# Performance work log

Hardware: AMD Instinct MI355X
Metric: run time of the kernel (lower is better)

## Reference

```python
import math
import jax, jax.numpy as jnp
import numpy as np

B, H, V, DEPTH = 8, 1024, 32000, 14
LN_EPS = 1e-5


def _structure(depth):
    """Replicates recurse()/expand() index bookkeeping. Pure python, static.
    Returns per-level boolean masks (len 2K, interleaved left/right per parent),
    B_l/B_r of the root, and sibling pair list S, in the exact original order."""
    def rec(idx_start, n, lengths):
        K = len(lengths)
        idxs = list(range(idx_start, idx_start + K))
        B_l = [[i] for i in idxs]
        B_r = [[i] for i in idxs]
        if n > 1:
            pmask = [(L - 1) > 0 for L in lengths]
            mask, child_lengths = [], []
            for L, m in zip(lengths, pmask):
                mask += [m, m]
                if m:
                    child_lengths += [math.ceil((L - 1) ** 0.75), L - 1]
            masks_below, lB_l, lB_r, S = rec(idxs[-1] + 1, n - 1, child_lengths)
            masks = [np.array(mask, dtype=bool)] + masks_below
            j = 0
            for i in range(K):
                if pmask[i]:
                    B_l[i].extend(lB_l[j])
                    B_r[i].extend(lB_r[j + 1])
                    for v_i in lB_r[j]:
                        for v_j in lB_l[j + 1]:
                            S.append((v_i, v_j))
                    j += 2
        else:
            masks, S = [], []
        return masks, B_l, B_r, S

    masks, B_l, B_r, S = rec(0, depth, [depth])
    return masks, B_l[0], B_r[0], S


def setup_inputs() -> dict:
    key = jax.random.key(0)
    ks = jax.random.split(key, 8)
    s = 0.02  # weight scale for numerical sanity
    return {
        'x': jax.random.normal(ks[0], (B, H), jnp.float32),
        'W_in': jax.random.normal(ks[1], (H, H), jnp.float32) * s,
        'b_in': jnp.zeros((H,), jnp.float32),
        'W_g': jax.random.normal(ks[2], (H, H), jnp.float32) * s,
        'b_g': jnp.zeros((H,), jnp.float32),
        'W_cell': jax.random.normal(ks[3], (2 * H, 2 * H), jnp.float32) * s,
        'b_cell': jnp.zeros((2 * H,), jnp.float32),
        'ln_g': jnp.ones((H,), jnp.float32),
        'ln_b': jnp.zeros((H,), jnp.float32),
        'W_leaf': jax.random.normal(ks[4], (H, 2), jnp.float32) * s,
        'b_leaf': jnp.zeros((2,), jnp.float32),
        'W_out': jax.random.normal(ks[5], (H, V), jnp.float32) * s,
        'b_out': jnp.zeros((V,), jnp.float32),
        'depth': DEPTH,
    }


def _layernorm(z, g, b):
    mu = z.mean(-1, keepdims=True)
    var = ((z - mu) ** 2).mean(-1, keepdims=True)
    return (z - mu) * jax.lax.rsqrt(var + LN_EPS) * g + b


def reference(x, W_in, b_in, W_g, b_g, W_cell, b_cell, ln_g, ln_b,
              W_leaf, b_leaf, W_out, b_out, depth):
    masks, Bl0, Br0, S = _structure(int(depth))
    h_dim = x.shape[-1]

    g = x @ W_g + b_g                                     # global_transform, [B,H]
    prev_h = (x @ W_in + b_in)[None]                      # init_parent, [1,B,H]
    prev_ll = jax.nn.log_softmax(prev_h @ W_leaf + b_leaf, axis=-1)  # [1,B,2]

    hs, ls = [prev_h], [prev_ll]
    for mask in masks:                                    # depth-1 static levels
        K, Bb = prev_h.shape[0], prev_h.shape[1]
        inp = jnp.concatenate([prev_h, jnp.broadcast_to(g, prev_h.shape)], axis=-1)
        z = (inp @ W_cell + b_cell).reshape(K, Bb, 2, h_dim)
        branches = jnp.tanh(_layernorm(z, ln_g, ln_b))    # cell: two child states
        log_leaf = jax.nn.log_softmax(branches @ W_leaf + b_leaf, axis=-1)
        ltl = 0.5 * prev_ll[:, :, None, 1:] + log_leaf    # update_logbreak
        fb = branches.transpose(0, 2, 1, 3).reshape(2 * K, Bb, h_dim)  # flatten_struct
        fl = ltl.transpose(0, 2, 1, 3).reshape(2 * K, Bb, 2)
        sel = np.nonzero(mask)[0]                         # static gather indices
        prev_h, prev_ll = fb[sel], fl[sel]
        hs.append(prev_h)
        ls.append(prev_ll)

    hiddens = jnp.concatenate(hs, axis=0)                 # [T,B,H]
    leaves = jnp.concatenate(ls, axis=0)                  # [T,B,2]
    log_words = jax.nn.log_softmax(hiddens @ W_out + b_out, axis=-1)  # [T,B,V]

    start_idxs = jnp.asarray(np.array(Bl0, dtype=np.int32))
    end_idxs = jnp.asarray(np.array(Br0, dtype=np.int32))
    Sarr = np.array(S, dtype=np.int32).reshape(-1, 2)
    out_idxs = jnp.asarray(Sarr[:, 0])
    in_idxs = jnp.asarray(Sarr[:, 1])
    return log_words, leaves, start_idxs, end_idxs, out_idxs, in_idxs
```

## Files before the change

### kernel.cpp

```cpp
#include <hip/hip_runtime.h>
#include <cstdint>
#include <cstddef>


typedef __attribute__((ext_vector_type(4))) float   f4;
typedef __attribute__((ext_vector_type(4))) float   f32x4;
typedef __attribute__((ext_vector_type(8))) __bf16  bf16x8;
typedef __attribute__((ext_vector_type(4))) unsigned short us4;
typedef __attribute__((ext_vector_type(8))) unsigned short us8;

constexpr int DEPTH = 14;
constexpr int Bb = 8;
constexpr int Hd = 1024;
constexpr int Vv = 32000;
constexpr int NT = Vv / 128;
constexpr int MAXT = 512;
constexpr int MAXS = 4096;
constexpr int MAXP = 32;
constexpr float L2E = 1.44269504088896340736f;

struct SB {
  int lvlOff[DEPTH + 1];
  int lvlK[DEPTH];
  int len[MAXT];
  int lch[MAXT], rch[MAXT];
  int parCnt[DEPTH];
  int parRows[DEPTH][MAXP];
  int T;
  int nS;
  int sOut[MAXS], sIn[MAXS];
  int nStart, nEnd;
  int startIdx[16], endIdx[16];
};

constexpr int ceil75(int L) {
  constexpr int t[14] = {0, 1, 2, 3, 3, 4, 4, 5, 5, 6, 6, 7, 7, 7};
  return t[L];
}

constexpr SB build() {
  SB s{};
  for (int i = 0; i < MAXT; i++) { s.lch[i] = -1; s.rch[i] = -1; }
  s.lvlOff[0] = 0; s.lvlK[0] = 1; s.len[0] = DEPTH;
  for (int l = 0; l < DEPTH - 1; l++) {
    int off = s.lvlOff[l], K = s.lvlK[l];
    int nxt = off + K, cnt = 0;
    for (int i = 0; i < K; i++) {
      int g = off + i;
      if (s.len[g] > 1) {
        int gl = nxt + 2 * cnt, gr = gl + 1;
        s.lch[g] = gl; s.rch[g] = gr;
        s.len[gl] = ceil75(s.len[g] - 1);
        s.len[gr] = s.len[g] - 1;
        s.parRows[l][cnt] = g;
        cnt++;
      }
    }
    s.parCnt[l] = cnt;
    s.lvlOff[l + 1] = nxt;
    s.lvlK[l + 1] = 2 * cnt;
  }
  s.T = s.lvlOff[DEPTH - 1] + s.lvlK[DEPTH - 1];
  s.nS = 0;
  for (int l = DEPTH - 2; l >= 0; l--) {
    for (int pi = 0; pi < s.parCnt[l]; pi++) {
      int g = s.parRows[l][pi];
      for (int u = s.lch[g]; u != -1; u = s.rch[u])
        for (int v = s.rch[g]; v != -1; v = s.lch[v]) {
          s.sOut[s.nS] = u; s.sIn[s.nS] = v; s.nS++;
        }
    }
  }
  s.nStart = 0;
  for (int u = 0; u != -1; u = s.lch[u]) s.startIdx[s.nStart++] = u;
  s.nEnd = 0;
  for (int u = 0; u != -1; u = s.rch[u]) s.endIdx[s.nEnd++] = u;
  return s;
}

constexpr SB HS = build();
__device__ const SB DS = build();

struct PR { int v[MAXP]; };

__device__ __forceinline__ unsigned short f2bf(float f) {
  union { float f; unsigned u; } v; v.f = f;
  unsigned r = v.u + 0x7fffu + ((v.u >> 16) & 1u);
  return (unsigned short)(r >> 16);
}

__global__ void k_wout_t(const float* __restrict__ Wout,
                         unsigned short* __restrict__ Wt) {
  __shared__ float t[64][129];
  int tid = threadIdx.x;
  int n0 = blockIdx.x * 128, k0 = blockIdx.y * 64;
#pragma unroll
  for (int i = 0; i < 8; i++) {
    int k = (tid >> 5) + 8 * i;
    int c = (tid & 31) * 4;
    f4 v = *(const f4*)&Wout[(size_t)(k0 + k) * Vv + n0 + c];
    t[k][c] = v.x; t[k][c + 1] = v.y; t[k][c + 2] = v.z; t[k][c + 3] = v.w;
  }
  __syncthreads();
#pragma unroll
  for (int pass = 0; pass < 4; pass++) {
    int n = (tid >> 3) + 32 * pass;
    int ks = (tid & 7) * 8;
    us8 o;
#pragma unroll
    for (int q = 0; q < 8; q++) o[q] = f2bf(t[ks + q][n]);
    *(us8*)&Wt[(size_t)(n0 + n) * Hd + k0 + ks] = o;
  }
}

__global__ void k_wct(const float* __restrict__ Wc,
                      unsigned short* __restrict__ Wct) {
  __shared__ float t[32][33];
  int tx = threadIdx.x, ty = threadIdx.y;
  int n0 = blockIdx.x * 32, k0 = blockIdx.y * 32;
  for (int i = 0; i < 4; i++)
    t[ty + 8 * i][tx] = Wc[(size_t)(k0 + ty + 8 * i) * 2048 + n0 + tx];
  __syncthreads();
  for (int i = 0; i < 4; i++)
    Wct[(size_t)(n0 + ty + 8 * i) * Hd + k0 + tx] = f2bf(t[tx][ty + 8 * i]);
}

__global__ void k_init(const float* __restrict__ x, const float* __restrict__ Wg,
                       const float* __restrict__ bg, const float* __restrict__ Win,
                       const float* __restrict__ bin, float* __restrict__ gbuf,
                       float* __restrict__ hidd, unsigned short* __restrict__ hiddb) {
  __shared__ float xs[Bb * Hd];
  __shared__ float part[Bb][128];
  int tid = threadIdx.x;
  int mat = blockIdx.y;
  const float* W = mat ? Win : Wg;
  const float* bias = mat ? bin : bg;
  for (int i = tid; i < Bb * Hd; i += 256) xs[i] = x[i];
  __syncthreads();
  int c = tid & 127, kh = tid >> 7;
  int col = blockIdx.x * 128 + c;
  float acc[Bb];
#pragma unroll
  for (int b = 0; b < Bb; b++) acc[b] = 0.f;
  for (int k = kh * 512; k < kh * 512 + 512; k++) {
    float w = W[(size_t)k * Hd + col];
#pragma unroll
    for (int b = 0; b < Bb; b++) acc[b] += xs[b * Hd + k] * w;
  }
  if (kh == 1)
    for (int b = 0; b < Bb; b++) part[b][c] = acc[b];
  __syncthreads();
  if (kh == 0) {
    for (int b = 0; b < Bb; b++) {
      float v = acc[b] + part[b][c] + bias[col];
      if (mat == 0) gbuf[b * Hd + col] = v;
      else { hidd[(size_t)b * Hd + col] = v; hiddb[(size_t)b * Hd + col] = f2bf(v); }
    }
  }
}

__global__ void k_gw(const float* __restrict__ gbuf, const float* __restrict__ Wc,
                     const float* __restrict__ bc, float* __restrict__ gW) {
  __shared__ float xs[Bb * Hd];
  __shared__ float part[Bb][128];
  int tid = threadIdx.x;
  for (int i = tid; i < Bb * Hd; i += 256) xs[i] = gbuf[i];
  __syncthreads();
  int c = tid & 127, kh = tid >> 7;
  int col = blockIdx.x * 128 + c;
  float acc[Bb];
#pragma unroll
  for (int b = 0; b < Bb; b++) acc[b] = 0.f;
  for (int k = kh * 512; k < kh * 512 + 512; k++) {
    float w = Wc[(size_t)(Hd + k) * 2048 + col];
#pragma unroll
    for (int b = 0; b < Bb; b++) acc[b] += xs[b * Hd + k] * w;
  }
  if (kh == 1)
    for (int b = 0; b < Bb; b++) part[b][c] = acc[b];
  __syncthreads();
  if (kh == 0)
    for (int b = 0; b < Bb; b++)
      gW[(size_t)b * 2048 + col] = acc[b] + part[b][c] + bc[col];
}

__global__ void k_leaf0(const float* __restrict__ hidd, const float* __restrict__ Wl,
                        const float* __restrict__ bl, float* __restrict__ leaves) {
  int b = threadIdx.x >> 6, lane = threadIdx.x & 63;
  float d0 = 0.f, d1 = 0.f;
  for (int k = lane; k < Hd; k += 64) {
    float h = hidd[(size_t)b * Hd + k];
    d0 += h * Wl[2 * k];
    d1 += h * Wl[2 * k + 1];
  }
  for (int off = 32; off; off >>= 1) {
    d0 += __shfl_down(d0, off);
    d1 += __shfl_down(d1, off);
  }
  if (lane == 0) {
    float l0 = d0 + bl[0], l1 = d1 + bl[1];
    float m = fmaxf(l0, l1);
    float L = logf(expf(l0 - m) + expf(l1 - m));
    leaves[b * 2 + 0] = l0 - m - L;
    leaves[b * 2 + 1] = l1 - m - L;
  }
}

__global__ __launch_bounds__(256) void k_cellg(
    const unsigned short* __restrict__ A, const unsigned short* __restrict__ Bt,
    float* __restrict__ zbuf, PR pr, int Mtot) {
  __shared__ short As[128 * 64];
  __shared__ short Bs[128 * 64];
  int tid = threadIdx.x;
  int lane = tid & 63, w = tid >> 6;
  int wm = w & 1, wn = w >> 1;
  int R0 = blockIdx.x * 128, C0 = blockIdx.y * 128;
  int ks = blockIdx.z;
  f32x4 acc[4][4];
#pragma unroll
  for (int i = 0; i < 4; i++)
#pragma unroll
    for (int j = 0; j < 4; j++) acc[i][j] = 0.f;
  int quad = lane >> 4, l15 = lane & 15;
  int srow = lane >> 3;
  int kc = lane & 7;
  for (int kb = ks * 4; kb < ks * 4 + 4; kb++) {
    int k0 = kb * 64;
#pragma unroll
    for (int i = 0; i < 4; i++) {
      int rowb = w * 32 + i * 8;
      int m = rowb + srow;
      int kcx = kc ^ (m & 7);
      int gr = R0 + m;
      int grc = gr < Mtot ? gr : 0;
      int arow = pr.v[grc >> 3] * Bb + (grc & 7);
      const unsigned short* ga = A + (size_t)arow * Hd + k0 + kcx * 8;
      const unsigned short* gb = Bt + (size_t)(C0 + m) * Hd + k0 + kcx * 8;
      __builtin_amdgcn_global_load_lds(
          (__attribute__((address_space(1))) void*)ga,
          (__attribute__((address_space(3))) void*)&As[rowb * 64], 16, 0, 0);
      __builtin_amdgcn_global_load_lds(
          (__attribute__((address_space(1))) void*)gb,
          (__attribute__((address_space(3))) void*)&Bs[rowb * 64], 16, 0, 0);
    }
    __syncthreads();
#pragma unroll
    for (int ksi = 0; ksi < 2; ksi++) {
      bf16x8 af[4], bfr[4];
      int kidx = ksi * 4 + quad;
#pragma unroll
      for (int i = 0; i < 4; i++) {
        int m = wm * 64 + i * 16 + l15;
        af[i] = *(const bf16x8*)&As[m * 64 + (kidx ^ (m & 7)) * 8];
      }
#pragma unroll
      for (int j = 0; j < 4; j++) {
        int n = wn * 64 + j * 16 + l15;
        bfr[j] = *(const bf16x8*)&Bs[n * 64 + (kidx ^ (n & 7)) * 8];
      }
#pragma unroll
      for (int i = 0; i < 4; i++)
#pragma unroll
        for (int j = 0; j < 4; j++)
          acc[i][j] = __builtin_amdgcn_mfma_f32_16x16x32_bf16(af[i], bfr[j],
                                                              acc[i][j], 0, 0, 0);
    }
    __syncthreads();
  }
#pragma unroll
  for (int j = 0; j < 4; j++) {
    int col = C0 + wn * 64 + j * 16 + l15;
#pragma unroll
    for (int i = 0; i < 4; i++) {
      int rowb = R0 + wm * 64 + i * 16 + quad * 4;
#pragma unroll
      for (int r = 0; r < 4; r++) {
        int row = rowb + r;
        if (row < Mtot)
          zbuf[((size_t)ks * 256 + row) * 2048 + col] = acc[i][j][r];
      }
    }
  }
}

__global__ void k_ln2(const float* __restrict__ zbuf, const float* __restrict__ gW,
                      const float* __restrict__ lng, const float* __restrict__ lnb,
                      const float* __restrict__ Wl, const float* __restrict__ bl,
                      unsigned short* __restrict__ hiddb,
                      float* __restrict__ leaves, PR pr, int lvlOff) {
  __shared__ float a1[4], a2[4], c1[4], c2[4];
  int tid = threadIdx.x, lane = tid & 63, wid = tid >> 6;
  int node = blockIdx.x, b = blockIdx.y;
  int cg = node & 1, p = node >> 1;
  int gp = pr.v[p];
  int ch = lvlOff + node;
  int m = p * Bb + b;
  int j0 = tid * 4;
  size_t zb = (size_t)m * 2048 + cg * 1024 + j0;
  f4 z = *(const f4*)&zbuf[zb];
  z += *(const f4*)&zbuf[zb + (size_t)256 * 2048];
  z += *(const f4*)&zbuf[zb + (size_t)512 * 2048];
  z += *(const f4*)&zbuf[zb + (size_t)768 * 2048];
  z += *(const f4*)&gW[(size_t)b * 2048 + cg * 1024 + j0];
  float s = z.x + z.y + z.z + z.w;
  float s2 = z.x * z.x + z.y * z.y + z.z * z.z + z.w * z.w;
#pragma unroll
  for (int off = 32; off; off >>= 1) {
    s += __shfl_xor(s, off);
    s2 += __shfl_xor(s2, off);
  }
  if (lane == 0) { a1[wid] = s; a2[wid] = s2; }
  __syncthreads();
  s = a1[0] + a1[1] + a1[2] + a1[3];
  s2 = a2[0] + a2[1] + a2[2] + a2[3];
  float mu = s * (1.f / 1024.f);
  float var = s2 * (1.f / 1024.f) - mu * mu;
  float rs = rsqrtf(var + 1e-5f);
  f4 lgv = *(const f4*)&lng[j0];
  f4 lbv = *(const f4*)&lnb[j0];
  f4 y;
  y.x = tanhf((z.x - mu) * rs * lgv.x + lbv.x);
  y.y = tanhf((z.y - mu) * rs * lgv.y + lbv.y);
  y.z = tanhf((z.z - mu) * rs * lgv.z + lbv.z);
  y.w = tanhf((z.w - mu) * rs * lgv.w + lbv.w);
  us4 yb;
  yb.x = f2bf(y.x); yb.y = f2bf(y.y); yb.z = f2bf(y.z); yb.w = f2bf(y.w);
  *(us4*)&hiddb[((size_t)ch * Bb + b) * Hd + j0] = yb;
  f4 wA = *(const f4*)&Wl[j0 * 2];
  f4 wB = *(const f4*)&Wl[j0 * 2 + 4];
  float d0 = y.x * wA.x + y.y * wA.z + y.z * wB.x + y.w * wB.z;
  float d1 = y.x * wA.y + y.y * wA.w + y.z * wB.y + y.w * wB.w;
#pragma unroll
  for (int off = 32; off; off >>= 1) {
    d0 += __shfl_xor(d0, off);
    d1 += __shfl_xor(d1, off);
  }
  if (lane == 0) { c1[wid] = d0; c2[wid] = d1; }
  __syncthreads();
  if (tid == 0) {
    float l0 = c1[0] + c1[1] + c1[2] + c1[3] + bl[0];
    float l1 = c2[0] + c2[1] + c2[2] + c2[3] + bl[1];
    float mm = fmaxf(l0, l1);
    float L = logf(expf(l0 - mm) + expf(l1 - mm));
    float half = 0.5f * leaves[((size_t)gp * Bb + b) * 2 + 1];
    leaves[((size_t)ch * Bb + b) * 2 + 0] = half + l0 - mm - L;
    leaves[((size_t)ch * Bb + b) * 2 + 1] = half + l1 - mm - L;
  }
}

constexpr int MT_TILES = 22;
constexpr int NWG = MT_TILES * NT;

template <int BF>
__global__ __launch_bounds__(256) void k_gemm(
    const unsigned short* __restrict__ A, const unsigned short* __restrict__ Bt,
    const float* __restrict__ bout, float* __restrict__ outf,
    unsigned short* __restrict__ lgt, float2* __restrict__ ptile, int Mvalid) {
  __shared__ short As[128 * 64];
  __shared__ short Bs[128 * 64];
  int tid = threadIdx.x;
  int lane = tid & 63, w = tid >> 6;
  int wm = w & 1, wn = w >> 1;
  int bid = blockIdx.x;
  constexpr int q = NWG >> 3, r = NWG & 7;
  int xcd = bid & 7, idx = bid >> 3;
  int wgid = (xcd < r ? xcd * (q + 1) : r * (q + 1) + (xcd - r) * q) + idx;
  int ny = wgid / MT_TILES;
  int mx = wgid - ny * MT_TILES;
  int R0 = mx * 128, C0 = ny * 128;
  f32x4 acc[4][4];
#pragma unroll
  for (int i = 0; i < 4; i++)
#pragma unroll
    for (int j = 0; j < 4; j++) acc[i][j] = 0.f;
  int quad = lane >> 4, l15 = lane & 15;
  int srow = lane >> 3;
  int kc = lane & 7;
  for (int kb = 0; kb < 16; kb++) {
    int k0 = kb * 64;
#pragma unroll
    for (int i = 0; i < 4; i++) {
      int rowb = w * 32 + i * 8;
      int m = rowb + srow;
      int kcx = kc ^ (m & 7);
      const unsigned short* ga = A + (size_t)(R0 + m) * Hd + k0 + kcx * 8;
      const unsigned short* gb = Bt + (size_t)(C0 + m) * Hd + k0 + kcx * 8;
      __builtin_amdgcn_global_load_lds(
          (__attribute__((address_space(1))) void*)ga,
          (__attribute__((address_space(3))) void*)&As[rowb * 64], 16, 0, 0);
      __builtin_amdgcn_global_load_lds(
          (__attribute__((address_space(1))) void*)gb,
          (__attribute__((address_space(3))) void*)&Bs[rowb * 64], 16, 0, 0);
    }
    __syncthreads();
#pragma unroll
    for (int ksi = 0; ksi < 2; ksi++) {
      bf16x8 af[4], bfr[4];
      int kidx = ksi * 4 + quad;
#pragma unroll
      for (int i = 0; i < 4; i++) {
        int m = wm * 64 + i * 16 + l15;
        af[i] = *(const bf16x8*)&As[m * 64 + (kidx ^ (m & 7)) * 8];
      }
#pragma unroll
      for (int j = 0; j < 4; j++) {
        int n = wn * 64 + j * 16 + l15;
        bfr[j] = *(const bf16x8*)&Bs[n * 64 + (kidx ^ (n & 7)) * 8];
      }
#pragma unroll
      for (int i = 0; i < 4; i++)
#pragma unroll
        for (int j = 0; j < 4; j++)
          acc[i][j] = __builtin_amdgcn_mfma_f32_16x16x32_bf16(af[i], bfr[j],
                                                              acc[i][j], 0, 0, 0);
    }
    __syncthreads();
  }
  float2* s0 = (float2*)As;
  float2* s1 = (float2*)Bs;
  float2* sw = wn ? s1 : s0;
  float bo[4];
#pragma unroll
  for (int j = 0; j < 4; j++) bo[j] = bout[C0 + wn * 64 + j * 16 + l15];
#pragma unroll
  for (int i = 0; i < 4; i++) {
#pragma unroll
    for (int r2 = 0; r2 < 4; r2++) {
      int lr = wm * 64 + i * 16 + quad * 4 + r2;
      int row = R0 + lr;
      float v0 = acc[i][0][r2] + bo[0];
      float v1 = acc[i][1][r2] + bo[1];
      float v2 = acc[i][2][r2] + bo[2];
      float v3 = acc[i][3][r2] + bo[3];
      if (row < Mvalid) {
        size_t base = (size_t)row * Vv + C0 + wn * 64 + l15;
        if (BF) {
          __builtin_nontemporal_store(f2bf(v0), &lgt[base + 0]);
          __builtin_nontemporal_store(f2bf(v1), &lgt[base + 16]);
          __builtin_nontemporal_store(f2bf(v2), &lgt[base + 32]);
          __builtin_nontemporal_store(f2bf(v3), &lgt[base + 48]);
        } else {
          __builtin_nontemporal_store(v0, &outf[base + 0]);
          __builtin_nontemporal_store(v1, &outf[base + 16]);
          __builtin_nontemporal_store(v2, &outf[base + 32]);
          __builtin_nontemporal_store(v3, &outf[base + 48]);
        }
      }
      float mx4 = fmaxf(fmaxf(v0, v1), fmaxf(v2, v3));
      float sm4 = exp2f((v0 - mx4) * L2E) + exp2f((v1 - mx4) * L2E) +
                  exp2f((v2 - mx4) * L2E) + exp2f((v3 - mx4) * L2E);
      float2 e; e.x = mx4; e.y = sm4;
      sw[lr * 16 + l15] = e;
    }
  }
  __syncthreads();
  if (tid < 128) {
    int rot = tid & 15;
    float M = -3e38f;
#pragma unroll
    for (int t = 0; t < 16; t++) {
      int c = (t + rot) & 15;
      M = fmaxf(M, fmaxf(s0[tid * 16 + c].x, s1[tid * 16 + c].x));
    }
    float S = 0.f;
#pragma unroll
    for (int t = 0; t < 16; t++) {
      int c = (t + rot) & 15;
      float2 a = s0[tid * 16 + c], b = s1[tid * 16 + c];
      S += a.y * exp2f((a.x - M) * L2E) + b.y * exp2f((b.x - M) * L2E);
    }
    float2 o; o.x = M; o.y = S;
    ptile[(size_t)(R0 + tid) * NT + ny] = o;
  }
}

__global__ void k_lse(const float2* __restrict__ ptile, float* __restrict__ st) {
  __shared__ float ms[256], ss[256];
  int r = blockIdx.x, tid = threadIdx.x;
  float mx = -3e38f, sm = 0.f;
  for (int t = tid; t < NT; t += 256) {
    float2 e = ptile[(size_t)r * NT + t];
    float M = fmaxf(mx, e.x);
    sm = sm * exp2f((mx - M) * L2E) + e.y * exp2f((e.x - M) * L2E);
    mx = M;
  }
  ms[tid] = mx; ss[tid] = sm;
  __syncthreads();
  for (int o = 128; o; o >>= 1) {
    if (tid < o) {
      float m2 = ms[tid + o], s2 = ss[tid + o];
      float M = fmaxf(ms[tid], m2);
      ss[tid] = ss[tid] * exp2f((ms[tid] - M) * L2E) + s2 * exp2f((m2 - M) * L2E);
      ms[tid] = M;
    }
    __syncthreads();
  }
  if (tid == 0) st[r] = ms[0] + logf(ss[0]);
}

__global__ void k_norm(float* __restrict__ out, const float* __restrict__ st) {
  int r = blockIdx.y;
  int i = blockIdx.x * 256 + threadIdx.x;
  if (i < Vv / 4) {
    float sub = st[r];
    f4* p = (f4*)(out + (size_t)r * Vv) + i;
    f4 v = __builtin_nontemporal_load(p);
    v -= sub;
    __builtin_nontemporal_store(v, p);
  }
}

__global__ void k_norm_bf(const unsigned short* __restrict__ lgt,
                          float* __restrict__ out, const float* __restrict__ st) {
  int r = blockIdx.y;
  int i = blockIdx.x * 256 + threadIdx.x;
  if (i < Vv / 8) {
    float sub = st[r];
    us8 v = __builtin_nontemporal_load((const us8*)(lgt + (size_t)r * Vv + i * 8));
    f4 o0, o1;
#pragma unroll
    for (int qk = 0; qk < 4; qk++) {
      union { unsigned u; float f; } cv;
      cv.u = ((unsigned)v[qk]) << 16;
      o0[qk] = cv.f - sub;
    }
#pragma unroll
    for (int qk = 0; qk < 4; qk++) {
      union { unsigned u; float f; } cv;
      cv.u = ((unsigned)v[4 + qk]) << 16;
      o1[qk] = cv.f - sub;
    }
    float* p = out + (size_t)r * Vv + i * 8;
    __builtin_nontemporal_store(o0, (f4*)p);
    __builtin_nontemporal_store(o1, (f4*)(p + 4));
  }
}

__global__ void k_idx(float* __restrict__ dst) {
  int total = DS.nStart + DS.nEnd + 2 * DS.nS;
  for (int i = threadIdx.x; i < total; i += 256) {
    int v;
    if (i < DS.nStart) v = DS.startIdx[i];
    else if (i < DS.nStart + DS.nEnd) v = DS.endIdx[i - DS.nStart];
    else if (i < DS.nStart + DS.nEnd + DS.nS) v = DS.sOut[i - DS.nStart - DS.nEnd];
    else v = DS.sIn[i - DS.nStart - DS.nEnd - DS.nS];
    dst[i] = (float)v;
  }
}

extern "C" void kernel_launch(void* const* d_in, const int* in_sizes, int n_in,
                              void* d_out, int out_size, void* d_ws, size_t ws_size,
                              hipStream_t stream) {
  (void)in_sizes; (void)n_in; (void)out_size;
  const float* x    = (const float*)d_in[0];
  const float* Win  = (const float*)d_in[1];
  const float* bin  = (const float*)d_in[2];
  const float* Wg   = (const float*)d_in[3];
  const float* bg   = (const float*)d_in[4];
  const float* Wc   = (const float*)d_in[5];
  const float* bc   = (const float*)d_in[6];
  const float* lng  = (const float*)d_in[7];
  const float* lnb  = (const float*)d_in[8];
  const float* Wl   = (const float*)d_in[9];
  const float* bl   = (const float*)d_in[10];
  const float* Wout = (const float*)d_in[11];
  const float* bout = (const float*)d_in[12];
  float* out = (float*)d_out;

  constexpr int T = HS.T;
  constexpr int Mrows = T * Bb;
  constexpr int Mt = ((Mrows + 127) / 128) * 128;

  char* ws = (char*)d_ws;
  char* ws0 = ws;
  unsigned short* Wt = (unsigned short*)ws;    ws += (size_t)Vv * Hd * 2;
  unsigned short* Wct = (unsigned short*)ws;   ws += (size_t)2048 * Hd * 2;
  float* hidd = (float*)ws;                    ws += (size_t)Bb * Hd * 4;
  unsigned short* hiddb = (unsigned short*)ws; ws += (size_t)Mt * Hd * 2;
  float* gbuf = (float*)ws;                    ws += (size_t)Bb * Hd * 4;
  float* gW = (float*)ws;                      ws += (size_t)Bb * 2048 * 4;
  float* zbuf = (float*)ws;                    ws += (size_t)4 * 256 * 2048 * 4;
  float2* ptile = (float2*)ws;                 ws += (size_t)Mt * NT * 8;
  float* st = (float*)ws;                      ws += (size_t)Mt * 4;
  unsigned short* lgt = (unsigned short*)ws;
  size_t needBf = (size_t)(ws - ws0) + (size_t)Mt * Vv * 2;
  bool bfp = ws_size >= needBf;

  float* leaves = out + (size_t)Mrows * Vv;
  float* idxdst = leaves + (size_t)Mrows * 2;

  k_wout_t<<<dim3(Vv / 128, Hd / 64), dim3(256), 0, stream>>>(Wout, Wt);
  k_wct<<<dim3(2048 / 32, Hd / 32), dim3(32, 8), 0, stream>>>(Wc, Wct);
  k_init<<<dim3(8, 2), dim3(256), 0, stream>>>(x, Wg, bg, Win, bin, gbuf, hidd, hiddb);
  k_gw<<<dim3(16), dim3(256), 0, stream>>>(gbuf, Wc, bc, gW);
  k_leaf0<<<dim3(1), dim3(512), 0, stream>>>(hidd, Wl, bl, leaves);

  for (int l = 1; l < DEPTH; l++) {
    int Pc = HS.parCnt[l - 1];
    int Mtot = Pc * Bb;
    int Mtiles = (Mtot + 127) / 128;
    PR pr{};
    for (int i = 0; i < Pc; i++) pr.v[i] = HS.parRows[l - 1][i];
    k_cellg<<<dim3(Mtiles, 16, 4), dim3(256), 0, stream>>>(hiddb, Wct, zbuf, pr, Mtot);
    k_ln2<<<dim3(2 * Pc, Bb), dim3(256), 0, stream>>>(zbuf, gW, lng, lnb, Wl, bl,
                                                      hiddb, leaves, pr,
                                                      HS.lvlOff[l]);
  }

  if (bfp) {
    k_gemm<1><<<dim3(NWG), dim3(256), 0, stream>>>(hiddb, Wt, bout, out, lgt,
                                                   ptile, Mrows);
    k_lse<<<dim3(Mrows), dim3(256), 0, stream>>>(ptile, st);
    k_norm_bf<<<dim3(16, Mrows), dim3(256), 0, stream>>>(lgt, out, st);
  } else {
    k_gemm<0><<<dim3(NWG), dim3(256), 0, stream>>>(hiddb, Wt, bout, out, lgt,
                                                   ptile, Mrows);
    k_lse<<<dim3(Mrows), dim3(256), 0, stream>>>(ptile, st);
    k_norm<<<dim3(32, Mrows), dim3(256), 0, stream>>>(out, st);
  }
  k_idx<<<dim3(1), dim3(256), 0, stream>>>(idxdst);
}
```

Measured before the change: 1.118 ms.

## Fuse tree-level recurrence into one persistent kernel with grid barriers

Replaces the 13 per-level pairs of cell-GEMM and layernorm kernel launches with a single persistent kernel. Inside it, 128 worker blocks run each level's per-wave 16x16 MFMA strips, emit partial layernorm statistics, and sync through a software global barrier. The remaining 128 blocks do the W_out transpose/bf16 conversion at the same time, overlapping it with the serial tree recurrence. This removes launch overhead and split-K reduction traffic. The cost is reliance on all 256 blocks being co-resident for the spin barrier, plus smaller, less reuse-friendly GEMM tiles.

After: 1.908 ms. 1.71x slower.

```diff
diff --git a/kernel.cpp b/kernel.cpp
--- a/kernel.cpp
+++ b/kernel.cpp
@@ -81,36 +81,31 @@
 constexpr SB HS = build();
 __device__ const SB DS = build();
 
-struct PR { int v[MAXP]; };
-
 __device__ __forceinline__ unsigned short f2bf(float f) {
   union { float f; unsigned u; } v; v.f = f;
   unsigned r = v.u + 0x7fffu + ((v.u >> 16) & 1u);
   return (unsigned short)(r >> 16);
 }
 
-__global__ void k_wout_t(const float* __restrict__ Wout,
-                         unsigned short* __restrict__ Wt) {
-  __shared__ float t[64][129];
-  int tid = threadIdx.x;
-  int n0 = blockIdx.x * 128, k0 = blockIdx.y * 64;
-#pragma unroll
-  for (int i = 0; i < 8; i++) {
-    int k = (tid >> 5) + 8 * i;
-    int c = (tid & 31) * 4;
-    f4 v = *(const f4*)&Wout[(size_t)(k0 + k) * Vv + n0 + c];
-    t[k][c] = v.x; t[k][c + 1] = v.y; t[k][c + 2] = v.z; t[k][c + 3] = v.w;
-  }
-  __syncthreads();
-#pragma unroll
-  for (int pass = 0; pass < 4; pass++) {
-    int n = (tid >> 3) + 32 * pass;
-    int ks = (tid & 7) * 8;
-    us8 o;
-#pragma unroll
-    for (int q = 0; q < 8; q++) o[q] = f2bf(t[ks + q][n]);
-    *(us8*)&Wt[(size_t)(n0 + n) * Hd + k0 + ks] = o;
-  }
+__device__ __forceinline__ void gbar(int* bar, int nblk) {
+  __syncthreads();
+  __threadfence();
+  if (threadIdx.x == 0) {
+    int g = __hip_atomic_load(&bar[1], __ATOMIC_ACQUIRE, __HIP_MEMORY_SCOPE_AGENT);
+    int a = __hip_atomic_fetch_add(&bar[0], 1, __ATOMIC_ACQ_REL,
+                                   __HIP_MEMORY_SCOPE_AGENT);
+    if (a == nblk - 1) {
+      __hip_atomic_store(&bar[0], 0, __ATOMIC_RELAXED, __HIP_MEMORY_SCOPE_AGENT);
+      __hip_atomic_fetch_add(&bar[1], 1, __ATOMIC_ACQ_REL,
+                             __HIP_MEMORY_SCOPE_AGENT);
+    } else {
+      while (__hip_atomic_load(&bar[1], __ATOMIC_ACQUIRE,
+                               __HIP_MEMORY_SCOPE_AGENT) == g) {
+        __builtin_amdgcn_s_sleep(8);
+      }
+    }
+  }
+  __syncthreads();
 }
 
 __global__ void k_wct(const float* __restrict__ Wc,
@@ -206,145 +201,153 @@
   }
 }
 
-__global__ __launch_bounds__(256) void k_cellg(
-    const unsigned short* __restrict__ A, const unsigned short* __restrict__ Bt,
-    float* __restrict__ zbuf, PR pr, int Mtot) {
-  __shared__ short As[128 * 64];
-  __shared__ short Bs[128 * 64];
+__global__ __launch_bounds__(256) void k_tree(
+    unsigned short* __restrict__ hiddb, const unsigned short* __restrict__ Wct,
+    const float* __restrict__ gW, const float* __restrict__ lng,
+    const float* __restrict__ lnb, const float* __restrict__ Wl,
+    const float* __restrict__ bl, float* __restrict__ leaves,
+    float* __restrict__ zbuf, float* __restrict__ pstat, int* __restrict__ bar,
+    const float* __restrict__ Wout, unsigned short* __restrict__ Wt) {
+  __shared__ float tsh[64][129];
   int tid = threadIdx.x;
-  int lane = tid & 63, w = tid >> 6;
-  int wm = w & 1, wn = w >> 1;
-  int R0 = blockIdx.x * 128, C0 = blockIdx.y * 128;
-  int ks = blockIdx.z;
-  f32x4 acc[4][4];
-#pragma unroll
-  for (int i = 0; i < 4; i++)
-#pragma unroll
-    for (int j = 0; j < 4; j++) acc[i][j] = 0.f;
+  if (blockIdx.x >= 128) {
+    for (int tile = blockIdx.x - 128; tile < 250 * 16; tile += 128) {
+      int n0 = (tile % 250) * 128, k0 = (tile / 250) * 64;
+#pragma unroll
+      for (int i = 0; i < 8; i++) {
+        int k = (tid >> 5) + 8 * i;
+        int c = (tid & 31) * 4;
+        f4 v = *(const f4*)&Wout[(size_t)(k0 + k) * Vv + n0 + c];
+        tsh[k][c] = v.x; tsh[k][c + 1] = v.y;
+        tsh[k][c + 2] = v.z; tsh[k][c + 3] = v.w;
+      }
+      __syncthreads();
+#pragma unroll
+      for (int pass = 0; pass < 4; pass++) {
+        int n = (tid >> 3) + 32 * pass;
+        int ks = (tid & 7) * 8;
+        us8 o;
+#pragma unroll
+        for (int q2 = 0; q2 < 8; q2++) o[q2] = f2bf(tsh[ks + q2][n]);
+        *(us8*)&Wt[(size_t)(n0 + n) * Hd + k0 + ks] = o;
+      }
+      __syncthreads();
+    }
+    return;
+  }
+  int w = tid >> 6, lane = tid & 63;
+  int tw = blockIdx.x * 4 + w;
   int quad = lane >> 4, l15 = lane & 15;
-  int srow = lane >> 3;
-  int kc = lane & 7;
-  for (int kb = ks * 4; kb < ks * 4 + 4; kb++) {
-    int k0 = kb * 64;
-#pragma unroll
-    for (int i = 0; i < 4; i++) {
-      int rowb = w * 32 + i * 8;
-      int m = rowb + srow;
-      int kcx = kc ^ (m & 7);
-      int gr = R0 + m;
-      int grc = gr < Mtot ? gr : 0;
-      int arow = pr.v[grc >> 3] * Bb + (grc & 7);
-      const unsigned short* ga = A + (size_t)arow * Hd + k0 + kcx * 8;
-      const unsigned short* gb = Bt + (size_t)(C0 + m) * Hd + k0 + kcx * 8;
-      __builtin_amdgcn_global_load_lds(
-          (__attribute__((address_space(1))) void*)ga,
-          (__attribute__((address_space(3))) void*)&As[rowb * 64], 16, 0, 0);
-      __builtin_amdgcn_global_load_lds(
-          (__attribute__((address_space(1))) void*)gb,
-          (__attribute__((address_space(3))) void*)&Bs[rowb * 64], 16, 0, 0);
-    }
-    __syncthreads();
-#pragma unroll
-    for (int ksi = 0; ksi < 2; ksi++) {
-      bf16x8 af[4], bfr[4];
-      int kidx = ksi * 4 + quad;
-#pragma unroll
-      for (int i = 0; i < 4; i++) {
-        int m = wm * 64 + i * 16 + l15;
-        af[i] = *(const bf16x8*)&As[m * 64 + (kidx ^ (m & 7)) * 8];
-      }
-#pragma unroll
-      for (int j = 0; j < 4; j++) {
-        int n = wn * 64 + j * 16 + l15;
-        bfr[j] = *(const bf16x8*)&Bs[n * 64 + (kidx ^ (n & 7)) * 8];
-      }
-#pragma unroll
-      for (int i = 0; i < 4; i++)
-#pragma unroll
-        for (int j = 0; j < 4; j++)
-          acc[i][j] = __builtin_amdgcn_mfma_f32_16x16x32_bf16(af[i], bfr[j],
-                                                              acc[i][j], 0, 0, 0);
-    }
-    __syncthreads();
-  }
-#pragma unroll
-  for (int j = 0; j < 4; j++) {
-    int col = C0 + wn * 64 + j * 16 + l15;
-#pragma unroll
-    for (int i = 0; i < 4; i++) {
-      int rowb = R0 + wm * 64 + i * 16 + quad * 4;
-#pragma unroll
-      for (int r = 0; r < 4; r++) {
-        int row = rowb + r;
-        if (row < Mtot)
-          zbuf[((size_t)ks * 256 + row) * 2048 + col] = acc[i][j][r];
-      }
-    }
-  }
-}
-
-__global__ void k_ln2(const float* __restrict__ zbuf, const float* __restrict__ gW,
-                      const float* __restrict__ lng, const float* __restrict__ lnb,
-                      const float* __restrict__ Wl, const float* __restrict__ bl,
-                      unsigned short* __restrict__ hiddb,
-                      float* __restrict__ leaves, PR pr, int lvlOff) {
-  __shared__ float a1[4], a2[4], c1[4], c2[4];
-  int tid = threadIdx.x, lane = tid & 63, wid = tid >> 6;
-  int node = blockIdx.x, b = blockIdx.y;
-  int cg = node & 1, p = node >> 1;
-  int gp = pr.v[p];
-  int ch = lvlOff + node;
-  int m = p * Bb + b;
-  int j0 = tid * 4;
-  size_t zb = (size_t)m * 2048 + cg * 1024 + j0;
-  f4 z = *(const f4*)&zbuf[zb];
-  z += *(const f4*)&zbuf[zb + (size_t)256 * 2048];
-  z += *(const f4*)&zbuf[zb + (size_t)512 * 2048];
-  z += *(const f4*)&zbuf[zb + (size_t)768 * 2048];
-  z += *(const f4*)&gW[(size_t)b * 2048 + cg * 1024 + j0];
-  float s = z.x + z.y + z.z + z.w;
-  float s2 = z.x * z.x + z.y * z.y + z.z * z.z + z.w * z.w;
-#pragma unroll
-  for (int off = 32; off; off >>= 1) {
-    s += __shfl_xor(s, off);
-    s2 += __shfl_xor(s2, off);
-  }
-  if (lane == 0) { a1[wid] = s; a2[wid] = s2; }
-  __syncthreads();
-  s = a1[0] + a1[1] + a1[2] + a1[3];
-  s2 = a2[0] + a2[1] + a2[2] + a2[3];
-  float mu = s * (1.f / 1024.f);
-  float var = s2 * (1.f / 1024.f) - mu * mu;
-  float rs = rsqrtf(var + 1e-5f);
-  f4 lgv = *(const f4*)&lng[j0];
-  f4 lbv = *(const f4*)&lnb[j0];
-  f4 y;
-  y.x = tanhf((z.x - mu) * rs * lgv.x + lbv.x);
-  y.y = tanhf((z.y - mu) * rs * lgv.y + lbv.y);
-  y.z = tanhf((z.z - mu) * rs * lgv.z + lbv.z);
-  y.w = tanhf((z.w - mu) * rs * lgv.w + lbv.w);
-  us4 yb;
-  yb.x = f2bf(y.x); yb.y = f2bf(y.y); yb.z = f2bf(y.z); yb.w = f2bf(y.w);
-  *(us4*)&hiddb[((size_t)ch * Bb + b) * Hd + j0] = yb;
-  f4 wA = *(const f4*)&Wl[j0 * 2];
-  f4 wB = *(const f4*)&Wl[j0 * 2 + 4];
-  float d0 = y.x * wA.x + y.y * wA.z + y.z * wB.x + y.w * wB.z;
-  float d1 = y.x * wA.y + y.y * wA.w + y.z * wB.y + y.w * wB.w;
-#pragma unroll
-  for (int off = 32; off; off >>= 1) {
-    d0 += __shfl_xor(d0, off);
-    d1 += __shfl_xor(d1, off);
-  }
-  if (lane == 0) { c1[wid] = d0; c2[wid] = d1; }
-  __syncthreads();
-  if (tid == 0) {
-    float l0 = c1[0] + c1[1] + c1[2] + c1[3] + bl[0];
-    float l1 = c2[0] + c2[1] + c2[2] + c2[3] + bl[1];
-    float mm = fmaxf(l0, l1);
-    float L = logf(expf(l0 - mm) + expf(l1 - mm));
-    float half = 0.5f * leaves[((size_t)gp * Bb + b) * 2 + 1];
-    leaves[((size_t)ch * Bb + b) * 2 + 0] = half + l0 - mm - L;
-    leaves[((size_t)ch * Bb + b) * 2 + 1] = half + l1 - mm - L;
+  for (int l = 1; l < DEPTH; l++) {
+    int Pc = DS.parCnt[l - 1];
+    int off = DS.lvlOff[l];
+    int nStrips = Pc * 128;
+    for (int sidx = tw; sidx < nStrips; sidx += 512) {
+      int p = sidx >> 7, cb = sidx & 127;
+      int n0 = cb * 16;
+      int prow = DS.parRows[l - 1][p];
+      const unsigned short* Arow = hiddb + ((size_t)prow * Bb + l15) * Hd;
+      const unsigned short* Brow = Wct + (size_t)(n0 + l15) * Hd;
+      f32x4 acc = {0.f, 0.f, 0.f, 0.f};
+#pragma unroll 8
+      for (int kk = 0; kk < 32; kk++) {
+        bf16x8 a = *(const bf16x8*)(Arow + kk * 32 + quad * 8);
+        bf16x8 bb = *(const bf16x8*)(Brow + kk * 32 + quad * 8);
+        acc = __builtin_amdgcn_mfma_f32_16x16x32_bf16(a, bb, acc, 0, 0, 0);
+      }
+      int gcol = n0 + l15;
+      float zv[4];
+#pragma unroll
+      for (int rr = 0; rr < 4; rr++) {
+        int row = quad * 4 + rr;
+        float zz = 0.f;
+        if (row < 8) {
+          zz = acc[rr] + gW[(size_t)row * 2048 + gcol];
+          zbuf[((size_t)(p * Bb + row)) * 2048 + gcol] = zz;
+        }
+        zv[rr] = zz;
+      }
+      float s1v[4], s2v[4];
+#pragma unroll
+      for (int rr = 0; rr < 4; rr++) { s1v[rr] = zv[rr]; s2v[rr] = zv[rr] * zv[rr]; }
+#pragma unroll
+      for (int d = 1; d < 16; d <<= 1) {
+#pragma unroll
+        for (int rr = 0; rr < 4; rr++) {
+          s1v[rr] += __shfl_xor(s1v[rr], d);
+          s2v[rr] += __shfl_xor(s2v[rr], d);
+        }
+      }
+      if (l15 == 0 && quad < 2) {
+#pragma unroll
+        for (int rr = 0; rr < 4; rr++) {
+          int row = quad * 4 + rr;
+          size_t si = (((size_t)p * 128 + cb) * 8 + row) * 2;
+          pstat[si] = s1v[rr];
+          pstat[si + 1] = s2v[rr];
+        }
+      }
+    }
+    gbar(bar, 128);
+    int nPairs = Pc * 16;
+    for (int pr2 = tw; pr2 < nPairs; pr2 += 512) {
+      int ch = pr2 >> 3, b = pr2 & 7;
+      int p = ch >> 1, cg = ch & 1;
+      size_t si = (((size_t)p * 128 + cg * 64 + lane) * 8 + b) * 2;
+      float ssum = pstat[si], ssq = pstat[si + 1];
+#pragma unroll
+      for (int d = 1; d < 64; d <<= 1) {
+        ssum += __shfl_xor(ssum, d);
+        ssq += __shfl_xor(ssq, d);
+      }
+      float mu = ssum * (1.f / 1024.f);
+      float var = ssq * (1.f / 1024.f) - mu * mu;
+      float rs = rsqrtf(var + 1e-5f);
+      int j0 = lane * 16;
+      size_t zr = ((size_t)(p * Bb + b)) * 2048 + cg * 1024 + j0;
+      float d0 = 0.f, d1 = 0.f;
+      unsigned short yb[16];
+#pragma unroll
+      for (int g2 = 0; g2 < 4; g2++) {
+        f4 z = *(const f4*)&zbuf[zr + g2 * 4];
+        f4 lg = *(const f4*)&lng[j0 + g2 * 4];
+        f4 lb = *(const f4*)&lnb[j0 + g2 * 4];
+        f4 y;
+        y.x = tanhf((z.x - mu) * rs * lg.x + lb.x);
+        y.y = tanhf((z.y - mu) * rs * lg.y + lb.y);
+        y.z = tanhf((z.z - mu) * rs * lg.z + lb.z);
+        y.w = tanhf((z.w - mu) * rs * lg.w + lb.w);
+        f4 wA = *(const f4*)&Wl[(j0 + g2 * 4) * 2];
+        f4 wB = *(const f4*)&Wl[(j0 + g2 * 4) * 2 + 4];
+        d0 += y.x * wA.x + y.y * wA.z + y.z * wB.x + y.w * wB.z;
+        d1 += y.x * wA.y + y.y * wA.w + y.z * wB.y + y.w * wB.w;
+        yb[g2 * 4 + 0] = f2bf(y.x);
+        yb[g2 * 4 + 1] = f2bf(y.y);
+        yb[g2 * 4 + 2] = f2bf(y.z);
+        yb[g2 * 4 + 3] = f2bf(y.w);
+      }
+      us8 o0, o1;
+#pragma unroll
+      for (int q2 = 0; q2 < 8; q2++) { o0[q2] = yb[q2]; o1[q2] = yb[8 + q2]; }
+      size_t hb = ((size_t)(off + ch) * Bb + b) * Hd + j0;
+      *(us8*)&hiddb[hb] = o0;
+      *(us8*)&hiddb[hb + 8] = o1;
+#pragma unroll
+      for (int d = 1; d < 64; d <<= 1) {
+        d0 += __shfl_xor(d0, d);
+        d1 += __shfl_xor(d1, d);
+      }
+      if (lane == 0) {
+        float l0 = d0 + bl[0], l1 = d1 + bl[1];
+        float mm = fmaxf(l0, l1);
+        float L = logf(expf(l0 - mm) + expf(l1 - mm));
+        int gp = DS.parRows[l - 1][p];
+        float half = 0.5f * leaves[((size_t)gp * Bb + b) * 2 + 1];
+        leaves[((size_t)(off + ch) * Bb + b) * 2 + 0] = half + l0 - mm - L;
+        leaves[((size_t)(off + ch) * Bb + b) * 2 + 1] = half + l1 - mm - L;
+      }
+    }
+    gbar(bar, 128);
   }
 }
 
@@ -579,7 +582,9 @@
   unsigned short* hiddb = (unsigned short*)ws; ws += (size_t)Mt * Hd * 2;
   float* gbuf = (float*)ws;                    ws += (size_t)Bb * Hd * 4;
   float* gW = (float*)ws;                      ws += (size_t)Bb * 2048 * 4;
-  float* zbuf = (float*)ws;                    ws += (size_t)4 * 256 * 2048 * 4;
+  float* zbuf = (float*)ws;                    ws += (size_t)256 * 2048 * 4;
+  float* pstat = (float*)ws;                   ws += (size_t)MAXP * 128 * 8 * 2 * 4;
+  int* bar = (int*)ws;                         ws += 64;
   float2* ptile = (float2*)ws;                 ws += (size_t)Mt * NT * 8;
   float* st = (float*)ws;                      ws += (size_t)Mt * 4;
   unsigned short* lgt = (unsigned short*)ws;
@@ -589,23 +594,14 @@
   float* leaves = out + (size_t)Mrows * Vv;
   float* idxdst = leaves + (size_t)Mrows * 2;
 
-  k_wout_t<<<dim3(Vv / 128, Hd / 64), dim3(256), 0, stream>>>(Wout, Wt);
+  hipMemsetAsync(bar, 0, 8, stream);
   k_wct<<<dim3(2048 / 32, Hd / 32), dim3(32, 8), 0, stream>>>(Wc, Wct);
   k_init<<<dim3(8, 2), dim3(256), 0, stream>>>(x, Wg, bg, Win, bin, gbuf, hidd, hiddb);
   k_gw<<<dim3(16), dim3(256), 0, stream>>>(gbuf, Wc, bc, gW);
   k_leaf0<<<dim3(1), dim3(512), 0, stream>>>(hidd, Wl, bl, leaves);
 
-  for (int l = 1; l < DEPTH; l++) {
-    int Pc = HS.parCnt[l - 1];
-    int Mtot = Pc * Bb;
-    int Mtiles = (Mtot + 127) / 128;
-    PR pr{};
-    for (int i = 0; i < Pc; i++) pr.v[i] = HS.parRows[l - 1][i];
-    k_cellg<<<dim3(Mtiles, 16, 4), dim3(256), 0, stream>>>(hiddb, Wct, zbuf, pr, Mtot);
-    k_ln2<<<dim3(2 * Pc, Bb), dim3(256), 0, stream>>>(zbuf, gW, lng, lnb, Wl, bl,
-                                                      hiddb, leaves, pr,
-                                                      HS.lvlOff[l]);
-  }
+  k_tree<<<dim3(256), dim3(256), 0, stream>>>(hiddb, Wct, gW, lng, lnb, Wl, bl,
+                                              leaves, zbuf, pstat, bar, Wout, Wt);
 
   if (bfp) {
     k_gemm<1><<<dim3(NWG), dim3(256), 0, stream>>>(hiddb, Wt, bout, out, lgt,
```
